# Optimization experiments

Hardware: AMD Instinct MI355X
Metric: run time of the kernel (lower is better)

The kernel has to match this reference:

```python
import jax, jax.numpy as jnp
import numpy as np


def _rotate_half(x):
    half = x.shape[-1] // 2
    x1, x2 = x[..., :half], x[..., half:]
    return jnp.concatenate([-x2, x1], axis=-1)


def setup_inputs() -> dict:
    key = jax.random.key(0)
    ks = jax.random.split(key, 7)
    B, T, D, H, Hd = 4, 2048, 1024, 16, 64
    x = jax.random.normal(ks[0], (B, T, D), dtype=jnp.float32)
    # RoPE tables (realistic: built from inv freqs)
    inv_freq = 1.0 / (10000.0 ** (jnp.arange(0, Hd, 2, dtype=jnp.float32) / Hd))
    pos = jnp.arange(T, dtype=jnp.float32)
    freqs = pos[:, None] * inv_freq[None, :]            # (T, Hd/2)
    emb = jnp.concatenate([freqs, freqs], axis=-1)       # (T, Hd)
    cos, sin = jnp.cos(emb), jnp.sin(emb)
    s = 1.0 / np.sqrt(D)
    w_q = jax.random.normal(ks[1], (D, D), dtype=jnp.float32) * s
    w_k = jax.random.normal(ks[2], (D, D), dtype=jnp.float32) * s
    w_v = jax.random.normal(ks[3], (D, D), dtype=jnp.float32) * s
    w_o = jax.random.normal(ks[4], (D, D), dtype=jnp.float32) * s
    return {"x": x, "cos": cos, "sin": sin, "w_q": w_q, "w_k": w_k, "w_v": w_v, "w_o": w_o}


def reference(x, cos, sin, w_q, w_k, w_v, w_o):
    B, T, D = x.shape
    H = 16
    Hd = D // H
    scale = Hd ** -0.5
    # nn.Linear(bias=False): y = x @ W.T
    q = (x @ w_q.T).reshape(B, T, H, Hd).transpose(0, 2, 1, 3)  # (B,H,T,Hd)
    k = (x @ w_k.T).reshape(B, T, H, Hd).transpose(0, 2, 1, 3)
    v = (x @ w_v.T).reshape(B, T, H, Hd).transpose(0, 2, 1, 3)
    c = cos[None, None, :, :]
    s = sin[None, None, :, :]
    q = q * c + _rotate_half(q) * s
    k = k * c + _rotate_half(k) * s
    scores = jnp.einsum('bhqd,bhkd->bhqk', q, k) * scale  # (B,H,T,T)
    causal = jnp.tril(jnp.ones((T, T), dtype=bool))
    scores = jnp.where(causal[None, None], scores, -jnp.inf)
    weights = jax.nn.softmax(scores, axis=-1)
    out = jnp.einsum('bhqk,bhkd->bhqd', weights, v)
    out = out.transpose(0, 2, 1, 3).reshape(B, T, D)
    return out @ w_o.T
```

## Files before the change

kernel.cpp:

```cpp
#include <hip/hip_runtime.h>
#include <stdint.h>

typedef __attribute__((ext_vector_type(8))) __bf16 bf16x8;
typedef __attribute__((ext_vector_type(4))) float floatx4;


__device__ __forceinline__ unsigned short f2bf(float f) {
    unsigned int u = __float_as_uint(f);
    u += 0x7FFFu + ((u >> 16) & 1u);
    return (unsigned short)(u >> 16);
}
__device__ __forceinline__ unsigned int pack2bf(float lo, float hi) {
    return (unsigned int)f2bf(lo) | ((unsigned int)f2bf(hi) << 16);
}
__device__ __forceinline__ unsigned int packtrunc(float lo, float hi) {
    return __builtin_amdgcn_perm(__float_as_uint(hi), __float_as_uint(lo), 0x07060302u);
}

__device__ __forceinline__ void gl_lds16(const void* g, void* l) {
    __builtin_amdgcn_global_load_lds(
        (const __attribute__((address_space(1))) void*)g,
        (__attribute__((address_space(3))) void*)l, 16, 0, 0);
}


__global__ void cvt_all(const float* __restrict__ x,  const float* __restrict__ wq,
                        const float* __restrict__ wk, const float* __restrict__ wv,
                        const float* __restrict__ wo,
                        unsigned short* __restrict__ xb,  unsigned short* __restrict__ wqb,
                        unsigned short* __restrict__ wkb, unsigned short* __restrict__ wvb,
                        unsigned short* __restrict__ wob) {
    int i = blockIdx.x * blockDim.x + threadIdx.x;
    const float* in; unsigned short* out; int idx;
    if (i < 2097152) { in = x; out = xb; idx = i; }
    else {
        int j = i - 2097152; int wsel = j >> 18; idx = j & 262143;
        in  = (wsel == 0) ? wq  : (wsel == 1) ? wk  : (wsel == 2) ? wv  : wo;
        out = (wsel == 0) ? wqb : (wsel == 1) ? wkb : (wsel == 2) ? wvb : wob;
    }
    float4 v = ((const float4*)in)[idx];
    ushort4 o;
    o.x = f2bf(v.x); o.y = f2bf(v.y); o.z = f2bf(v.z); o.w = f2bf(v.w);
    ((ushort4*)out)[idx] = o;
}


template<int MODE>
__global__ __launch_bounds__(256, 2)
void gemm_bt(const unsigned short* __restrict__ A,
             const unsigned short* __restrict__ Wq,
             const unsigned short* __restrict__ Wk,
             const float* __restrict__ cosp,
             const float* __restrict__ sinp,
             unsigned short* __restrict__ outq,
             unsigned short* __restrict__ outk,
             unsigned short* __restrict__ outvt,
             float* __restrict__ outf)
{
    constexpr int K = 1024;
    __shared__ __align__(16) unsigned short As[128 * 32];
    __shared__ __align__(16) unsigned short Bs[128 * 32];

    const int t    = threadIdx.x;
    const int w    = t >> 6;
    const int lane = t & 63;
    const int c    = lane & 15;
    const int quad = lane >> 4;
    const int wr   = w >> 1, wc = w & 1;

    const int m0 = blockIdx.x * 128;
    int which, n0;
    const unsigned short* W;
    if constexpr (MODE == 0) {
        which = blockIdx.y >> 3;
        n0    = (blockIdx.y & 7) * 128;
        W     = which ? Wk : Wq;
    } else {
        which = 0;
        n0    = blockIdx.y * 128;
        W     = Wq;
    }

    const int srow = t >> 2;
    const int scol = (t & 3) * 8;
    const unsigned short* ga0 = A + (size_t)(m0 + srow) * K + scol;
    const unsigned short* ga1 = A + (size_t)(m0 + srow + 64) * K + scol;
    const unsigned short* gb0 = W + (size_t)(n0 + srow) * K + scol;
    const unsigned short* gb1 = W + (size_t)(n0 + srow + 64) * K + scol;
    void* lA0 = (char*)As + t * 16;
    void* lA1 = (char*)As + 4096 + t * 16;
    void* lB0 = (char*)Bs + t * 16;
    void* lB1 = (char*)Bs + 4096 + t * 16;

    floatx4 acc[4][4] = {};

    const int arow = wr * 64;
    const int brow = wc * 64;

    for (int k0 = 0; k0 < K; k0 += 32) {
        __syncthreads();
        gl_lds16(ga0 + k0, lA0);
        gl_lds16(ga1 + k0, lA1);
        gl_lds16(gb0 + k0, lB0);
        gl_lds16(gb1 + k0, lB1);
        __syncthreads();
        bf16x8 af[4], bfr[4];
        #pragma unroll
        for (int mi = 0; mi < 4; mi++)
            af[mi] = *(const bf16x8*)&As[(arow + mi * 16 + c) * 32 + quad * 8];
        #pragma unroll
        for (int ni = 0; ni < 4; ni++)
            bfr[ni] = *(const bf16x8*)&Bs[(brow + ni * 16 + c) * 32 + quad * 8];
        if constexpr (MODE == 2) {
            #pragma unroll
            for (int mi = 0; mi < 4; mi++)
                #pragma unroll
                for (int ni = 0; ni < 4; ni++)
                    acc[mi][ni] = __builtin_amdgcn_mfma_f32_16x16x32_bf16(
                        af[mi], bfr[ni], acc[mi][ni], 0, 0, 0);
        } else {
            #pragma unroll
            for (int mi = 0; mi < 4; mi++)
                #pragma unroll
                for (int ni = 0; ni < 4; ni++)
                    acc[mi][ni] = __builtin_amdgcn_mfma_f32_16x16x32_bf16(
                        bfr[ni], af[mi], acc[mi][ni], 0, 0, 0);
        }
    }

    if constexpr (MODE == 1) {
        #pragma unroll
        for (int mi = 0; mi < 4; mi++) {
            int m = m0 + wr * 64 + mi * 16 + c;
            #pragma unroll
            for (int ni = 0; ni < 4; ni++) {
                int n = n0 + wc * 64 + ni * 16 + quad * 4;
                *(floatx4*)&outf[(size_t)m * 1024 + n] = acc[mi][ni];
            }
        }
    } else if constexpr (MODE == 2) {
        const int hh = (n0 + wc * 64) >> 6;
        #pragma unroll
        for (int mi = 0; mi < 4; mi++) {
            int t0 = m0 + wr * 64 + mi * 16 + quad * 4;
            int b = t0 >> 11, tt0 = t0 & 2047;
            #pragma unroll
            for (int ni = 0; ni < 4; ni++) {
                int d = ni * 16 + c;
                uint2 pk;
                pk.x = pack2bf(acc[mi][ni][0], acc[mi][ni][1]);
                pk.y = pack2bf(acc[mi][ni][2], acc[mi][ni][3]);
                *(uint2*)&outvt[((size_t)((b * 16 + hh) * 64 + d)) * 2048 + tt0] = pk;
            }
        }
    } else {
        const int hh = (n0 + wc * 64) >> 6;
        unsigned short* dst = which ? outk : outq;
        const float scale = which ? 1.0f : (0.125f * 1.44269504088896f);
        #pragma unroll
        for (int mi = 0; mi < 4; mi++) {
            int m = m0 + wr * 64 + mi * 16 + c;
            int b = m >> 11, tt = m & 2047;
            size_t obase = ((size_t)(b * 16 + hh) * 2048 + tt) * 64;
            #pragma unroll
            for (int ni = 0; ni < 4; ni++) {
                int d0 = ni * 16 + quad * 4;
                float4 cv = *(const float4*)&cosp[tt * 64 + d0];
                float4 sv = *(const float4*)&sinp[tt * 64 + d0];
                float ca[4] = {cv.x, cv.y, cv.z, cv.w};
                float sa[4] = {sv.x, sv.y, sv.z, sv.w};
                float vq[4];
                #pragma unroll
                for (int r = 0; r < 4; r++) {
                    float pr  = acc[mi][ni ^ 2][r];
                    float rot = (ni & 2) ? pr : -pr;
                    vq[r] = (acc[mi][ni][r] * ca[r] + rot * sa[r]) * scale;
                }
                uint2 pk;
                pk.x = pack2bf(vq[0], vq[1]);
                pk.y = pack2bf(vq[2], vq[3]);
                *(uint2*)&dst[obase + d0] = pk;
            }
        }
    }
}

__global__ __launch_bounds__(256)
void flash_attn(const unsigned short* __restrict__ Q,
                const unsigned short* __restrict__ Kg,
                const unsigned short* __restrict__ Vt,
                unsigned short* __restrict__ O)
{
    __shared__ __align__(16) unsigned short Ks[2][64 * 64];
    __shared__ __align__(16) unsigned short Vs[2][64 * 64];
    __shared__ __align__(16) unsigned short Ps[4 * 16 * 64];

    const int t    = threadIdx.x;
    const int w    = t >> 6;
    const int lane = t & 63;
    const int c    = lane & 15;
    const int quad = lane >> 4;

    const int bh = blockIdx.x;
    const int b  = bh >> 4, h = bh & 15;

    const unsigned short* qp = Q  + (size_t)bh * 2048 * 64;
    const unsigned short* kp = Kg + (size_t)bh * 2048 * 64;
    const unsigned short* vp = Vt + (size_t)bh * 64 * 2048;

    const int srow = t >> 3;
    const int sj   = (t & 7) ^ (srow & 7);
    unsigned short* pw = Ps + w * (16 * 64);

    for (int pp = 0; pp < 2; pp++) {
        const int qi = pp ? (31 - (int)blockIdx.y) : (int)blockIdx.y;
        const int q0 = qi * 64;
        const int qb = q0 + w * 16;

        bf16x8 qf[2];
        #pragma unroll
        for (int dc = 0; dc < 2; dc++)
            qf[dc] = *(const bf16x8*)&qp[(size_t)(qb + c) * 64 + dc * 32 + quad * 8];

        floatx4 o[4] = {};
        float lpart = 0.f;

        __syncthreads();
        #pragma unroll
        for (int ch = 0; ch < 2; ch++) {
            int kr = ch * 32 + srow;
            gl_lds16(kp + (size_t)kr * 64 + sj * 8, (char*)&Ks[0][0] + ch * 4096 + t * 16);
            gl_lds16(vp + (size_t)kr * 2048 + sj * 8, (char*)&Vs[0][0] + ch * 4096 + t * 16);
        }

        const int iters = qi + 1;
        for (int it = 0; it < iters; it++) {
            const int cur = it & 1;
            const int kt0 = it * 64;
            __syncthreads();
            if (it + 1 < iters) {
                const int kt1 = kt0 + 64;
                #pragma unroll
                for (int ch = 0; ch < 2; ch++) {
                    int kr = ch * 32 + srow;
                    gl_lds16(kp + (size_t)(kt1 + kr) * 64 + sj * 8,
                             (char*)&Ks[cur ^ 1][0] + ch * 4096 + t * 16);
                    gl_lds16(vp + (size_t)kr * 2048 + kt1 + sj * 8,
                             (char*)&Vs[cur ^ 1][0] + ch * 4096 + t * 16);
                }
            }
            const unsigned short* KsC = &Ks[cur][0];
            const unsigned short* VsC = &Vs[cur][0];

            floatx4 s[4] = {};
            #pragma unroll
            for (int dc = 0; dc < 2; dc++) {
                const int phys = (dc * 4 + quad) ^ (c & 7);
                #pragma unroll
                for (int mt = 0; mt < 4; mt++) {
                    bf16x8 kb = *(const bf16x8*)&KsC[(mt * 16 + c) * 64 + phys * 8];
                    s[mt] = __builtin_amdgcn_mfma_f32_16x16x32_bf16(kb, qf[dc], s[mt], 0, 0, 0);
                }
            }

            if (it == iters - 1) {
                #pragma unroll
                for (int mt = 0; mt < 4; mt++) {
                    int keyb = kt0 + mt * 16 + quad * 4;
                    #pragma unroll
                    for (int r = 0; r < 4; r++)
                        if (keyb + r > qb + c) s[mt][r] = -1e30f;
                }
            }

            uint2 pk[4];
            #pragma unroll
            for (int mt = 0; mt < 4; mt++) {
                float p0 = __builtin_amdgcn_exp2f(s[mt][0]);
                float p1 = __builtin_amdgcn_exp2f(s[mt][1]);
                float p2 = __builtin_amdgcn_exp2f(s[mt][2]);
                float p3 = __builtin_amdgcn_exp2f(s[mt][3]);
                lpart += (p0 + p1) + (p2 + p3);
                pk[mt].x = packtrunc(p0, p1);
                pk[mt].y = packtrunc(p2, p3);
            }

            #pragma unroll
            for (int mt = 0; mt < 4; mt++) {
                int blk = (mt * 2 + (quad >> 1)) ^ (c & 7);
                *(uint2*)&pw[c * 64 + blk * 8 + (quad & 1) * 4] = pk[mt];
            }

            #pragma unroll
            for (int kc = 0; kc < 2; kc++) {
                const int phys = (kc * 4 + quad) ^ (c & 7);
                bf16x8 ap = *(const bf16x8*)&pw[c * 64 + phys * 8];
                #pragma unroll
                for (int ni = 0; ni < 4; ni++) {
                    bf16x8 vb = *(const bf16x8*)&VsC[(ni * 16 + c) * 64 + phys * 8];
                    o[ni] = __builtin_amdgcn_mfma_f32_16x16x32_bf16(ap, vb, o[ni], 0, 0, 0);
                }
            }
        }

        float l = lpart;
        l += __shfl_xor(l, 16);
        l += __shfl_xor(l, 32);
        float li = __builtin_amdgcn_rcpf(l);
        #pragma unroll
        for (int r = 0; r < 4; r++) {
            float linv = __shfl(li, quad * 4 + r);
            int qrow = qb + quad * 4 + r;
            size_t base = ((size_t)(b * 2048 + qrow)) * 1024 + h * 64;
            #pragma unroll
            for (int ni = 0; ni < 4; ni++)
                O[base + ni * 16 + c] = f2bf(o[ni][r] * linv);
        }
    }
}


extern "C" void kernel_launch(void* const* d_in, const int* in_sizes, int n_in,
                              void* d_out, int out_size, void* d_ws, size_t ws_size,
                              hipStream_t stream) {
    const float* x    = (const float*)d_in[0];
    const float* cosp = (const float*)d_in[1];
    const float* sinp = (const float*)d_in[2];
    const float* wq   = (const float*)d_in[3];
    const float* wk   = (const float*)d_in[4];
    const float* wv   = (const float*)d_in[5];
    const float* wo   = (const float*)d_in[6];

    char* ws = (char*)d_ws;
    const size_t MB = 1024 * 1024;
    unsigned short* xb   = (unsigned short*)(ws + 0);
    unsigned short* attn = (unsigned short*)(ws + 0);
    unsigned short* wqb  = (unsigned short*)(ws + 16 * MB);
    unsigned short* wkb  = (unsigned short*)(ws + 18 * MB);
    unsigned short* wvb  = (unsigned short*)(ws + 20 * MB);
    unsigned short* wob  = (unsigned short*)(ws + 22 * MB);
    unsigned short* qbuf = (unsigned short*)(ws + 24 * MB);
    unsigned short* kbuf = (unsigned short*)(ws + 40 * MB);
    unsigned short* vtb  = (unsigned short*)(ws + 56 * MB);

    cvt_all<<<dim3(12288), 256, 0, stream>>>(x, wq, wk, wv, wo,
                                             xb, wqb, wkb, wvb, wob);

    gemm_bt<0><<<dim3(64, 16), 256, 0, stream>>>(xb, wqb, wkb, cosp, sinp,
                                                 qbuf, kbuf, nullptr, nullptr);
    gemm_bt<2><<<dim3(64, 8), 256, 0, stream>>>(xb, wvb, nullptr, nullptr, nullptr,
                                                nullptr, nullptr, vtb, nullptr);

    flash_attn<<<dim3(64, 16), 256, 0, stream>>>(qbuf, kbuf, vtb, attn);

    gemm_bt<1><<<dim3(64, 8), 256, 0, stream>>>(attn, wob, nullptr, nullptr, nullptr,
                                                nullptr, nullptr, nullptr, (float*)d_out);
}
```

Measured before the change: 262.4 us.

## Split key tiles across waves with 128-key blocks and LDS cross-wave reduction

The flash-attention kernel now gives every wave all 64 query rows and a 32-key slice of a 128-key tile, instead of each wave owning 16 query rows over a 64-key tile. This halves the number of loop iterations and barriers, and each K and V fragment loaded from shared memory is reused across four query tiles. The price is an end-of-block reduction of the partial O accumulators and row sums through shared memory, a larger LDS footprint (about 80KB) that may lower occupancy, and more accumulator registers. The output store is also widened to packed 64-bit writes.

```diff
diff --git a/kernel.cpp b/kernel.cpp
--- a/kernel.cpp
+++ b/kernel.cpp
@@ -191,9 +191,10 @@
                 const unsigned short* __restrict__ Vt,
                 unsigned short* __restrict__ O)
 {
-    __shared__ __align__(16) unsigned short Ks[2][64 * 64];
-    __shared__ __align__(16) unsigned short Vs[2][64 * 64];
-    __shared__ __align__(16) unsigned short Ps[4 * 16 * 64];
+    __shared__ __align__(16) unsigned short SMEM[40960];
+    unsigned short* Ks = SMEM;
+    unsigned short* Vs = SMEM + 16384;
+    unsigned short* Ps = SMEM + 32768;
 
     const int t    = threadIdx.x;
     const int w    = t >> 6;
@@ -208,113 +209,161 @@
     const unsigned short* kp = Kg + (size_t)bh * 2048 * 64;
     const unsigned short* vp = Vt + (size_t)bh * 64 * 2048;
 
-    const int srow = t >> 3;
-    const int sj   = (t & 7) ^ (srow & 7);
-    unsigned short* pw = Ps + w * (16 * 64);
+    const int krow = t >> 3;
+    const int kblk = (t & 7) ^ (krow & 7);
+    const int vrow = t >> 4;
+    const int vblk = (t & 15) ^ (vrow & 15);
+    unsigned short* pw = Ps + w * (64 * 32);
+
+    const int c7  = c & 7;
+    const int c3  = (c >> 1) & 3;
 
     for (int pp = 0; pp < 2; pp++) {
         const int qi = pp ? (31 - (int)blockIdx.y) : (int)blockIdx.y;
         const int q0 = qi * 64;
-        const int qb = q0 + w * 16;
-
-        bf16x8 qf[2];
-        #pragma unroll
-        for (int dc = 0; dc < 2; dc++)
-            qf[dc] = *(const bf16x8*)&qp[(size_t)(qb + c) * 64 + dc * 32 + quad * 8];
-
-        floatx4 o[4] = {};
-        float lpart = 0.f;
+
+        bf16x8 qf[4][2];
+        #pragma unroll
+        for (int qt = 0; qt < 4; qt++)
+            #pragma unroll
+            for (int dc = 0; dc < 2; dc++)
+                qf[qt][dc] = *(const bf16x8*)&qp[(size_t)(q0 + qt * 16 + c) * 64 + dc * 32 + quad * 8];
+
+        floatx4 o[4][4] = {};
+        float lp[4] = {};
 
         __syncthreads();
         #pragma unroll
-        for (int ch = 0; ch < 2; ch++) {
-            int kr = ch * 32 + srow;
-            gl_lds16(kp + (size_t)kr * 64 + sj * 8, (char*)&Ks[0][0] + ch * 4096 + t * 16);
-            gl_lds16(vp + (size_t)kr * 2048 + sj * 8, (char*)&Vs[0][0] + ch * 4096 + t * 16);
-        }
-
-        const int iters = qi + 1;
+        for (int ch = 0; ch < 4; ch++) {
+            gl_lds16(kp + (size_t)(ch * 32 + krow) * 64 + kblk * 8,
+                     (char*)Ks + ch * 4096 + t * 16);
+            gl_lds16(vp + (size_t)(ch * 16 + vrow) * 2048 + vblk * 8,
+                     (char*)Vs + ch * 4096 + t * 16);
+        }
+
+        const int iters = (qi >> 1) + 1;
         for (int it = 0; it < iters; it++) {
             const int cur = it & 1;
-            const int kt0 = it * 64;
+            const int kt0 = it * 128;
             __syncthreads();
             if (it + 1 < iters) {
-                const int kt1 = kt0 + 64;
-                #pragma unroll
-                for (int ch = 0; ch < 2; ch++) {
-                    int kr = ch * 32 + srow;
-                    gl_lds16(kp + (size_t)(kt1 + kr) * 64 + sj * 8,
-                             (char*)&Ks[cur ^ 1][0] + ch * 4096 + t * 16);
-                    gl_lds16(vp + (size_t)kr * 2048 + kt1 + sj * 8,
-                             (char*)&Vs[cur ^ 1][0] + ch * 4096 + t * 16);
+                const int kt1 = kt0 + 128;
+                #pragma unroll
+                for (int ch = 0; ch < 4; ch++) {
+                    gl_lds16(kp + (size_t)(kt1 + ch * 32 + krow) * 64 + kblk * 8,
+                             (char*)Ks + (cur ^ 1) * 8192 * 2 + ch * 4096 + t * 16);
+                    gl_lds16(vp + (size_t)(ch * 16 + vrow) * 2048 + kt1 + vblk * 8,
+                             (char*)Vs + (cur ^ 1) * 8192 * 2 + ch * 4096 + t * 16);
                 }
             }
-            const unsigned short* KsC = &Ks[cur][0];
-            const unsigned short* VsC = &Vs[cur][0];
-
-            floatx4 s[4] = {};
+            const unsigned short* KsC = Ks + cur * 8192;
+            const unsigned short* VsC = Vs + cur * 8192;
+
+            floatx4 s[2][4] = {};
             #pragma unroll
             for (int dc = 0; dc < 2; dc++) {
-                const int phys = (dc * 4 + quad) ^ (c & 7);
-                #pragma unroll
-                for (int mt = 0; mt < 4; mt++) {
-                    bf16x8 kb = *(const bf16x8*)&KsC[(mt * 16 + c) * 64 + phys * 8];
-                    s[mt] = __builtin_amdgcn_mfma_f32_16x16x32_bf16(kb, qf[dc], s[mt], 0, 0, 0);
+                const int phys = (dc * 4 + quad) ^ c7;
+                bf16x8 kf[2];
+                #pragma unroll
+                for (int kt = 0; kt < 2; kt++)
+                    kf[kt] = *(const bf16x8*)&KsC[(w * 32 + kt * 16 + c) * 64 + phys * 8];
+                #pragma unroll
+                for (int kt = 0; kt < 2; kt++)
+                    #pragma unroll
+                    for (int qt = 0; qt < 4; qt++)
+                        s[kt][qt] = __builtin_amdgcn_mfma_f32_16x16x32_bf16(
+                            kf[kt], qf[qt][dc], s[kt][qt], 0, 0, 0);
+            }
+
+            if (it == iters - 1) {
+                #pragma unroll
+                for (int kt = 0; kt < 2; kt++) {
+                    int keyb = kt0 + w * 32 + kt * 16 + quad * 4;
+                    #pragma unroll
+                    for (int qt = 0; qt < 4; qt++) {
+                        int qrow = q0 + qt * 16 + c;
+                        #pragma unroll
+                        for (int r = 0; r < 4; r++)
+                            if (keyb + r > qrow) s[kt][qt][r] = -1e30f;
+                    }
                 }
             }
 
-            if (it == iters - 1) {
-                #pragma unroll
-                for (int mt = 0; mt < 4; mt++) {
-                    int keyb = kt0 + mt * 16 + quad * 4;
+            #pragma unroll
+            for (int kt = 0; kt < 2; kt++) {
+                const int physw = (kt * 2 + (quad >> 1)) ^ c3;
+                #pragma unroll
+                for (int qt = 0; qt < 4; qt++) {
+                    float p0 = __builtin_amdgcn_exp2f(s[kt][qt][0]);
+                    float p1 = __builtin_amdgcn_exp2f(s[kt][qt][1]);
+                    float p2 = __builtin_amdgcn_exp2f(s[kt][qt][2]);
+                    float p3 = __builtin_amdgcn_exp2f(s[kt][qt][3]);
+                    lp[qt] += (p0 + p1) + (p2 + p3);
+                    uint2 pk;
+                    pk.x = packtrunc(p0, p1);
+                    pk.y = packtrunc(p2, p3);
+                    *(uint2*)&pw[(qt * 16 + c) * 32 + physw * 8 + (quad & 1) * 4] = pk;
+                }
+            }
+
+            {
+                const int physp = quad ^ c3;
+                const int physv = (w * 4 + quad) ^ c;
+                bf16x8 vf[4], pf[4];
+                #pragma unroll
+                for (int dt = 0; dt < 4; dt++)
+                    vf[dt] = *(const bf16x8*)&VsC[(dt * 16 + c) * 128 + physv * 8];
+                #pragma unroll
+                for (int qt = 0; qt < 4; qt++)
+                    pf[qt] = *(const bf16x8*)&pw[(qt * 16 + c) * 32 + physp * 8];
+                #pragma unroll
+                for (int qt = 0; qt < 4; qt++)
                     #pragma unroll
-                    for (int r = 0; r < 4; r++)
-                        if (keyb + r > qb + c) s[mt][r] = -1e30f;
-                }
-            }
-
-            uint2 pk[4];
-            #pragma unroll
-            for (int mt = 0; mt < 4; mt++) {
-                float p0 = __builtin_amdgcn_exp2f(s[mt][0]);
-                float p1 = __builtin_amdgcn_exp2f(s[mt][1]);
-                float p2 = __builtin_amdgcn_exp2f(s[mt][2]);
-                float p3 = __builtin_amdgcn_exp2f(s[mt][3]);
-                lpart += (p0 + p1) + (p2 + p3);
-                pk[mt].x = packtrunc(p0, p1);
-                pk[mt].y = packtrunc(p2, p3);
-            }
-
-            #pragma unroll
-            for (int mt = 0; mt < 4; mt++) {
-                int blk = (mt * 2 + (quad >> 1)) ^ (c & 7);
-                *(uint2*)&pw[c * 64 + blk * 8 + (quad & 1) * 4] = pk[mt];
-            }
-
-            #pragma unroll
-            for (int kc = 0; kc < 2; kc++) {
-                const int phys = (kc * 4 + quad) ^ (c & 7);
-                bf16x8 ap = *(const bf16x8*)&pw[c * 64 + phys * 8];
-                #pragma unroll
-                for (int ni = 0; ni < 4; ni++) {
-                    bf16x8 vb = *(const bf16x8*)&VsC[(ni * 16 + c) * 64 + phys * 8];
-                    o[ni] = __builtin_amdgcn_mfma_f32_16x16x32_bf16(ap, vb, o[ni], 0, 0, 0);
-                }
-            }
-        }
-
-        float l = lpart;
-        l += __shfl_xor(l, 16);
-        l += __shfl_xor(l, 32);
-        float li = __builtin_amdgcn_rcpf(l);
-        #pragma unroll
-        for (int r = 0; r < 4; r++) {
-            float linv = __shfl(li, quad * 4 + r);
-            int qrow = qb + quad * 4 + r;
-            size_t base = ((size_t)(b * 2048 + qrow)) * 1024 + h * 64;
-            #pragma unroll
-            for (int ni = 0; ni < 4; ni++)
-                O[base + ni * 16 + c] = f2bf(o[ni][r] * linv);
+                    for (int dt = 0; dt < 4; dt++)
+                        o[qt][dt] = __builtin_amdgcn_mfma_f32_16x16x32_bf16(
+                            vf[dt], pf[qt], o[qt][dt], 0, 0, 0);
+            }
+        }
+
+        __syncthreads();
+        float* red  = (float*)SMEM;
+        float* lred = (float*)(SMEM + 32768);
+
+        #pragma unroll
+        for (int qt = 0; qt < 4; qt++) {
+            int row = qt * 16 + c;
+            #pragma unroll
+            for (int dt = 0; dt < 4; dt++)
+                *(floatx4*)&red[w * 4096 + row * 64 + ((dt * 4 + quad) ^ c) * 4] = o[qt][dt];
+        }
+        float ls[4];
+        #pragma unroll
+        for (int qt = 0; qt < 4; qt++) {
+            float l = lp[qt];
+            l += __shfl_xor(l, 16);
+            l += __shfl_xor(l, 32);
+            ls[qt] = l;
+        }
+        float lsel = (quad == 0) ? ls[0] : (quad == 1) ? ls[1] : (quad == 2) ? ls[2] : ls[3];
+        lred[w * 64 + quad * 16 + c] = lsel;
+        __syncthreads();
+
+        const int row = w * 16 + c;
+        floatx4 of[4] = {};
+        #pragma unroll
+        for (int j = 0; j < 4; j++)
+            #pragma unroll
+            for (int dt = 0; dt < 4; dt++)
+                of[dt] += *(const floatx4*)&red[j * 4096 + row * 64 + ((dt * 4 + quad) ^ c) * 4];
+        float l = lred[row] + lred[64 + row] + lred[128 + row] + lred[192 + row];
+        float linv = __builtin_amdgcn_rcpf(l);
+        size_t base = ((size_t)(b * 2048 + q0 + row)) * 1024 + h * 64;
+        #pragma unroll
+        for (int dt = 0; dt < 4; dt++) {
+            uint2 pk;
+            pk.x = pack2bf(of[dt][0] * linv, of[dt][1] * linv);
+            pk.y = pack2bf(of[dt][2] * linv, of[dt][3] * linv);
+            *(uint2*)&O[base + dt * 16 + quad * 4] = pk;
         }
     }
 }
```

Measured after the change: 291.0 us. 1.11x slower.
